# Kernel optimization log

Hardware: AMD Instinct MI355X
Metric: run time of the kernel (lower is better)

## Reference

```python
import jax, jax.numpy as jnp
import numpy as np

EMBED_DIM = 256
NUM_HEADS = 8
WINDOW = 64
HEAD_DIM = EMBED_DIM // NUM_HEADS


def setup_inputs() -> dict:
    key = jax.random.key(0)
    k_x, k_w, k_ow = jax.random.split(key, 3)
    B, S, E = 2, 4096, EMBED_DIM
    x = jax.random.normal(k_x, (B, S, E), dtype=jnp.float32)
    # nn.MultiheadAttention params: packed in_proj (q,k,v) and out_proj
    bound = 1.0 / np.sqrt(E)
    in_proj_w = jax.random.uniform(k_w, (3 * E, E), jnp.float32, -bound, bound)
    in_proj_b = jnp.zeros((3 * E,), jnp.float32)
    out_w = jax.random.uniform(k_ow, (E, E), jnp.float32, -bound, bound)
    out_b = jnp.zeros((E,), jnp.float32)
    return {"x": x, "in_proj_w": in_proj_w, "in_proj_b": in_proj_b,
            "out_w": out_w, "out_b": out_b}


def reference(x, in_proj_w, in_proj_b, out_w, out_b):
    B, S, E = x.shape
    H, D = NUM_HEADS, HEAD_DIM
    # packed qkv projection (torch Linear: y = x @ W^T + b)
    qkv = jnp.einsum('bse,fe->bsf', x, in_proj_w) + in_proj_b  # [B,S,3E]
    q, k, v = jnp.split(qkv, 3, axis=-1)
    q = q.reshape(B, S, H, D).transpose(0, 2, 1, 3)  # [B,H,S,D]
    k = k.reshape(B, S, H, D).transpose(0, 2, 1, 3)
    v = v.reshape(B, S, H, D).transpose(0, 2, 1, 3)
    scale = 1.0 / jnp.sqrt(jnp.asarray(D, x.dtype))
    scores = jnp.einsum('bhqd,bhkd->bhqk', q * scale, k)  # [B,H,S,S]
    idx = jnp.arange(S)
    band = jnp.abs(idx[:, None] - idx[None, :]) <= WINDOW  # [S,S]
    neg = jnp.asarray(-1e9, scores.dtype)
    scores = jnp.where(band[None, None, :, :], scores, neg)
    attn = jax.nn.softmax(scores, axis=-1)
    out = jnp.einsum('bhqk,bhkd->bhqd', attn, v)  # [B,H,S,D]
    out = out.transpose(0, 2, 1, 3).reshape(B, S, E)
    return jnp.einsum('bse,fe->bsf', out, out_w) + out_b
```

## Files before the change

### kernel.cpp

```cpp
#include <hip/hip_runtime.h>
#include <hip/hip_bf16.h>

#define S_LEN 4096
#define EMB   256
#define NHEAD 8
#define HDIM  32
#define WIN   64
#define BATCH 2

typedef __attribute__((ext_vector_type(8))) short short8;
typedef __attribute__((ext_vector_type(4))) float floatx4;
typedef __attribute__((ext_vector_type(4))) unsigned short ushort4v;
typedef unsigned short u16;
typedef unsigned int   u32;

static __device__ __forceinline__ u32 bf16_rn(float x) {
    u32 u = __float_as_uint(x);
    return (u + 0x7FFFu + ((u >> 16) & 1u)) >> 16;
}

static __device__ __forceinline__ void gload16(const u16* g, u16* l) {
    __builtin_amdgcn_global_load_lds(
        (const __attribute__((address_space(1))) void*)g,
        (__attribute__((address_space(3))) void*)l, 16, 0, 0);
}

#define NX4 524288
#define NW4 49152
#define NO4 16384

__global__ __launch_bounds__(256) void convert_kernel(
    const float* __restrict__ X, const float* __restrict__ Wi, const float* __restrict__ Wo,
    u16* __restrict__ Xh, u16* __restrict__ Xl,
    u16* __restrict__ Wih, u16* __restrict__ Wil,
    u16* __restrict__ Woh, u16* __restrict__ Wol)
{
    const int i = blockIdx.x * 256 + threadIdx.x;
    const float* src; u16 *dh, *dl; int off;
    if (i < NX4)            { src = X;  dh = Xh;  dl = Xl;  off = i; }
    else if (i < NX4 + NW4) { src = Wi; dh = Wih; dl = Wil; off = i - NX4; }
    else                    { src = Wo; dh = Woh; dl = Wol; off = i - NX4 - NW4; }
    const float4 v = *(const float4*)(src + (size_t)off * 4);
    ushort4v h, l;
    {
        u32 hb;
        hb = bf16_rn(v.x); h.x = (u16)hb; l.x = (u16)bf16_rn(v.x - __uint_as_float(hb << 16));
        hb = bf16_rn(v.y); h.y = (u16)hb; l.y = (u16)bf16_rn(v.y - __uint_as_float(hb << 16));
        hb = bf16_rn(v.z); h.z = (u16)hb; l.z = (u16)bf16_rn(v.z - __uint_as_float(hb << 16));
        hb = bf16_rn(v.w); h.w = (u16)hb; l.w = (u16)bf16_rn(v.w - __uint_as_float(hb << 16));
    }
    *(ushort4v*)(dh + (size_t)off * 4) = h;
    *(ushort4v*)(dl + (size_t)off * 4) = l;
}

#define BK 32

__global__ __launch_bounds__(256) void qkv_proj_kernel(
    const u16* __restrict__ Xh, const u16* __restrict__ Xl,
    const u16* __restrict__ Wh, const u16* __restrict__ Wl,
    const float* __restrict__ bias,
    u16* __restrict__ Qh, u16* __restrict__ Ql,
    u16* __restrict__ Kh, u16* __restrict__ Kl,
    u16* __restrict__ Vh)
{
    __shared__ __align__(16) u16 SA[2][2][128 * BK];
    __shared__ __align__(16) u16 SB[2][2][64 * BK];

    const int tid = threadIdx.x;
    const int wg0 = blockIdx.y * 12 + blockIdx.x;
    const int wg = (wg0 & 7) * 96 + (wg0 >> 3);
    const int n0 = (wg % 12) * 64, m0 = (wg / 12) * 128;
    const int lane = tid & 63, wv = tid >> 6;
    const int lm = lane & 15, kq = lane >> 4;
    const int gr = lane >> 2;
    const int gc = ((lane & 3) ^ ((lane >> 3) & 3)) * 8;
    const int swz = (lm >> 1) & 3;
    const int wm = (wv >> 1) * 64, wn = (wv & 1) * 32;

    auto stage = [&](int buf, int k0) {
#pragma unroll
        for (int cc = 0; cc < 2; ++cc) {
            const int c = 2 * wv + cc;
            const size_t grow = (size_t)(m0 + 16 * c + gr) * EMB + k0 + gc;
            gload16(Xh + grow, &SA[buf][0][c * 512]);
            gload16(Xl + grow, &SA[buf][1][c * 512]);
        }
        const size_t brow = (size_t)(n0 + 16 * wv + gr) * EMB + k0 + gc;
        gload16(Wh + brow, &SB[buf][0][wv * 512]);
        gload16(Wl + brow, &SB[buf][1][wv * 512]);
    };

    floatx4 acc[4][2] = {};
    stage(0, 0);
    __syncthreads();
    int cur = 0;
    for (int t = 0; t < 8; ++t) {
        if (t < 7) stage(cur ^ 1, (t + 1) * 32);
        short8 a_h[4], a_l[4], b_h[2], b_l[2];
#pragma unroll
        for (int mt = 0; mt < 4; ++mt) {
            const int ro = (wm + mt * 16 + lm) * BK + (kq ^ swz) * 8;
            a_h[mt] = *(const short8*)&SA[cur][0][ro];
            a_l[mt] = *(const short8*)&SA[cur][1][ro];
        }
#pragma unroll
        for (int nt = 0; nt < 2; ++nt) {
            const int ro = (wn + nt * 16 + lm) * BK + (kq ^ swz) * 8;
            b_h[nt] = *(const short8*)&SB[cur][0][ro];
            b_l[nt] = *(const short8*)&SB[cur][1][ro];
        }
#pragma unroll
        for (int mt = 0; mt < 4; ++mt)
#pragma unroll
            for (int nt = 0; nt < 2; ++nt) {
                acc[mt][nt] = __builtin_amdgcn_mfma_f32_16x16x32_bf16(a_h[mt], b_h[nt], acc[mt][nt], 0, 0, 0);
                acc[mt][nt] = __builtin_amdgcn_mfma_f32_16x16x32_bf16(a_h[mt], b_l[nt], acc[mt][nt], 0, 0, 0);
                acc[mt][nt] = __builtin_amdgcn_mfma_f32_16x16x32_bf16(a_l[mt], b_h[nt], acc[mt][nt], 0, 0, 0);
            }
        __syncthreads();
        cur ^= 1;
    }
#pragma unroll
    for (int nt = 0; nt < 2; ++nt) {
        const int f = n0 + wn + nt * 16 + lm;
        const int which = f >> 8;
        const int hh = (f & 255) >> 5, d = f & 31;
        u16* dh = (which == 0) ? Qh : ((which == 1) ? Kh : Vh);
        u16* dl = (which == 0) ? Ql : Kl;
        const float sc2 = (which == 0) ? 0.17677669529663687f : 1.0f;
        const float bf = bias[f];
#pragma unroll
        for (int mt = 0; mt < 4; ++mt)
#pragma unroll
            for (int r = 0; r < 4; ++r) {
                const int m = m0 + wm + mt * 16 + kq * 4 + r;
                const int b = m >> 12, s = m & (S_LEN - 1);
                const size_t idx = (((size_t)b * NHEAD + hh) * S_LEN + s) * HDIM + d;
                const float val = (acc[mt][nt][r] + bf) * sc2;
                const u32 hbits = bf16_rn(val);
                dh[idx] = (u16)hbits;
                if (which != 2)
                    dl[idx] = (u16)bf16_rn(val - __uint_as_float(hbits << 16));
            }
    }
}

__global__ __launch_bounds__(256) void out_proj_kernel(
    const u16* __restrict__ Ahp, const u16* __restrict__ Alp,
    const u16* __restrict__ Wh, const u16* __restrict__ Wl,
    const float* __restrict__ bias, float* __restrict__ C)
{
    __shared__ __align__(16) u16 SA[2][2][64 * BK];
    __shared__ __align__(16) u16 SB[2][2][64 * BK];
    const int tid = threadIdx.x;
    const int wg0 = blockIdx.y * 4 + blockIdx.x;
    const int wg = (wg0 & 7) * 64 + (wg0 >> 3);
    const int n0 = (wg & 3) * 64, m0 = (wg >> 2) * 64;
    const int lane = tid & 63, wv = tid >> 6;
    const int lm = lane & 15, kq = lane >> 4;
    const int gr = lane >> 2;
    const int gc = ((lane & 3) ^ ((lane >> 3) & 3)) * 8;
    const int swz = (lm >> 1) & 3;
    const int wm = (wv >> 1) * 32, wn = (wv & 1) * 32;

    auto stage = [&](int buf, int k0) {
        const size_t arow = (size_t)(m0 + 16 * wv + gr) * EMB + k0 + gc;
        gload16(Ahp + arow, &SA[buf][0][wv * 512]);
        gload16(Alp + arow, &SA[buf][1][wv * 512]);
        const size_t brow = (size_t)(n0 + 16 * wv + gr) * EMB + k0 + gc;
        gload16(Wh + brow, &SB[buf][0][wv * 512]);
        gload16(Wl + brow, &SB[buf][1][wv * 512]);
    };

    floatx4 acc[2][2] = {};
    stage(0, 0);
    __syncthreads();
    int cur = 0;
    for (int t = 0; t < 8; ++t) {
        if (t < 7) stage(cur ^ 1, (t + 1) * 32);
        short8 a_h[2], a_l[2], b_h[2], b_l[2];
#pragma unroll
        for (int mt = 0; mt < 2; ++mt) {
            const int ro = (wm + mt * 16 + lm) * BK + (kq ^ swz) * 8;
            a_h[mt] = *(const short8*)&SA[cur][0][ro];
            a_l[mt] = *(const short8*)&SA[cur][1][ro];
        }
#pragma unroll
        for (int nt = 0; nt < 2; ++nt) {
            const int ro = (wn + nt * 16 + lm) * BK + (kq ^ swz) * 8;
            b_h[nt] = *(const short8*)&SB[cur][0][ro];
            b_l[nt] = *(const short8*)&SB[cur][1][ro];
        }
#pragma unroll
        for (int mt = 0; mt < 2; ++mt)
#pragma unroll
            for (int nt = 0; nt < 2; ++nt) {
                acc[mt][nt] = __builtin_amdgcn_mfma_f32_16x16x32_bf16(a_h[mt], b_h[nt], acc[mt][nt], 0, 0, 0);
                acc[mt][nt] = __builtin_amdgcn_mfma_f32_16x16x32_bf16(a_h[mt], b_l[nt], acc[mt][nt], 0, 0, 0);
                acc[mt][nt] = __builtin_amdgcn_mfma_f32_16x16x32_bf16(a_l[mt], b_h[nt], acc[mt][nt], 0, 0, 0);
            }
        __syncthreads();
        cur ^= 1;
    }
#pragma unroll
    for (int nt = 0; nt < 2; ++nt) {
        const int f = n0 + wn + nt * 16 + lm;
        const float bf = bias[f];
#pragma unroll
        for (int mt = 0; mt < 2; ++mt)
#pragma unroll
            for (int r = 0; r < 4; ++r) {
                const int m = m0 + wm + mt * 16 + kq * 4 + r;
                C[(size_t)m * EMB + f] = acc[mt][nt][r] + bf;
            }
    }
}

#define AKS 40
#define AVS 200

__global__ __launch_bounds__(256) void local_attn_kernel(
    const u16* __restrict__ Qhg, const u16* __restrict__ Qlg,
    const u16* __restrict__ Khg, const u16* __restrict__ Klg,
    const u16* __restrict__ Vhg,
    u16* __restrict__ Abh, u16* __restrict__ Abl)
{
    __shared__ __align__(16) u16 sKh[192 * AKS], sKl[192 * AKS];
    __shared__ __align__(16) u16 sVt[32 * AVS];

    const int tid = threadIdx.x;
    const int q0 = blockIdx.x * 64;
    const int h = blockIdx.y, b = blockIdx.z;
    const int jmin = max(0, q0 - WIN);
    const int jmax = min(S_LEN - 1, q0 + 63 + WIN);
    const int nk = jmax - jmin + 1;
    const size_t bhS = ((size_t)b * NHEAD + h) * S_LEN;
    const size_t qoff = (bhS + q0) * HDIM;
    const size_t koff = (bhS + jmin) * HDIM;

    const int lane = tid & 63, wv = tid >> 6;
    const int lm = lane & 15, quad = lane >> 4;
    const int qbase = wv * 16;

    const short8 qh = *(const short8*)(Qhg + qoff + (size_t)(qbase + lm) * HDIM + quad * 8);
    const short8 ql = *(const short8*)(Qlg + qoff + (size_t)(qbase + lm) * HDIM + quad * 8);

    const int srow = tid >> 2, sc = tid & 3;
#pragma unroll
    for (int r = 0; r < 3; ++r) {
        const int t = srow + r * 64;
        const int tc = min(t, nk - 1);
        const size_t go = koff + (size_t)tc * HDIM + sc * 8;
        *(short8*)&sKh[t * AKS + sc * 8] = *(const short8*)(Khg + go);
        *(short8*)&sKl[t * AKS + sc * 8] = *(const short8*)(Klg + go);
    }
#pragma unroll
    for (int r = 0; r < 3; ++r) {
        const int t = srow + r * 64;
        const int tc = min(t, nk - 1);
        const short8 v = *(const short8*)(Vhg + koff + (size_t)tc * HDIM + sc * 8);
        const int d0 = sc * 8;
#pragma unroll
        for (int j = 0; j < 8; ++j)
            sVt[(d0 + j) * AVS + t] = (u16)v[j];
    }
    __syncthreads();

    const int tb = max(0, ((wv >> 1) << 1) + (min(q0 - WIN, 0) >> 4));

    floatx4 sacc[10];
#pragma unroll
    for (int i = 0; i < 10; ++i) {
        const int nt = tb + i;
        const short8 kh = *(const short8*)&sKh[(nt * 16 + lm) * AKS + quad * 8];
        const short8 kl = *(const short8*)&sKl[(nt * 16 + lm) * AKS + quad * 8];
        floatx4 a = {};
        a = __builtin_amdgcn_mfma_f32_16x16x32_bf16(kh, qh, a, 0, 0, 0);
        a = __builtin_amdgcn_mfma_f32_16x16x32_bf16(kh, ql, a, 0, 0, 0);
        a = __builtin_amdgcn_mfma_f32_16x16x32_bf16(kl, qh, a, 0, 0, 0);
        sacc[i] = a;
    }

    const int qr = q0 + qbase + lm;
    float mx = -1e30f;
#pragma unroll
    for (int i = 0; i < 10; ++i) {
        const int sbase = (tb + i) * 16 + quad * 4;
#pragma unroll
        for (int r = 0; r < 4; ++r) {
            const int slot = sbase + r;
            const int keyg = jmin + slot;
            const bool valid = (slot < nk) && (keyg >= qr - WIN) && (keyg <= qr + WIN);
            const float sv = valid ? sacc[i][r] : -1e30f;
            sacc[i][r] = sv;
            mx = fmaxf(mx, sv);
        }
    }
    mx = fmaxf(mx, __shfl_xor(mx, 16));
    mx = fmaxf(mx, __shfl_xor(mx, 32));

    float l = 0.f;
    u32 pk_[20];
#pragma unroll
    for (int i = 0; i < 10; ++i) {
        const float p0 = __expf(sacc[i][0] - mx);
        const float p1 = __expf(sacc[i][1] - mx);
        const float p2 = __expf(sacc[i][2] - mx);
        const float p3 = __expf(sacc[i][3] - mx);
        l += (p0 + p1) + (p2 + p3);
        pk_[2 * i]     = bf16_rn(p0) | (bf16_rn(p1) << 16);
        pk_[2 * i + 1] = bf16_rn(p2) | (bf16_rn(p3) << 16);
    }
    l += __shfl_xor(l, 16);
    l += __shfl_xor(l, 32);
    const float rl = 1.f / l;

    const int kb = tb >> 1;
    floatx4 oacc[2] = {};
#pragma unroll
    for (int i = 0; i < 5; ++i) {
        const int ks = kb + i;
        uint4 aw;
        aw.x = pk_[4 * i + 0];
        aw.y = pk_[4 * i + 1];
        aw.z = pk_[4 * i + 2];
        aw.w = pk_[4 * i + 3];
        const short8 ap = *(const short8*)&aw;
        const int sb = ks * 32 + quad * 4;
        const uint2 e0 = *(const uint2*)&sVt[lm * AVS + sb];
        const uint2 o0 = *(const uint2*)&sVt[lm * AVS + sb + 16];
        const uint2 e1 = *(const uint2*)&sVt[(16 + lm) * AVS + sb];
        const uint2 o1 = *(const uint2*)&sVt[(16 + lm) * AVS + sb + 16];
        uint4 bw0; bw0.x = e0.x; bw0.y = e0.y; bw0.z = o0.x; bw0.w = o0.y;
        uint4 bw1; bw1.x = e1.x; bw1.y = e1.y; bw1.z = o1.x; bw1.w = o1.y;
        const short8 bv0 = *(const short8*)&bw0;
        const short8 bv1 = *(const short8*)&bw1;
        oacc[0] = __builtin_amdgcn_mfma_f32_16x16x32_bf16(ap, bv0, oacc[0], 0, 0, 0);
        oacc[1] = __builtin_amdgcn_mfma_f32_16x16x32_bf16(ap, bv1, oacc[1], 0, 0, 0);
    }

    float rlr[4];
#pragma unroll
    for (int r = 0; r < 4; ++r) rlr[r] = __shfl(rl, quad * 4 + r);
#pragma unroll
    for (int nt = 0; nt < 2; ++nt)
#pragma unroll
        for (int r = 0; r < 4; ++r) {
            const int qrow = qbase + quad * 4 + r;
            const float o = oacc[nt][r] * rlr[r];
            const u32 hb = bf16_rn(o);
            const size_t idx = ((size_t)b * S_LEN + q0 + qrow) * EMB + h * HDIM + nt * 16 + lm;
            Abh[idx] = (u16)hb;
            Abl[idx] = (u16)bf16_rn(o - __uint_as_float(hb << 16));
        }
}

extern "C" void kernel_launch(void* const* d_in, const int* in_sizes, int n_in,
                              void* d_out, int out_size, void* d_ws, size_t ws_size,
                              hipStream_t stream) {
    const float* x  = (const float*)d_in[0];
    const float* wi = (const float*)d_in[1];
    const float* bi = (const float*)d_in[2];
    const float* wo = (const float*)d_in[3];
    const float* bo = (const float*)d_in[4];
    float* out = (float*)d_out;

    const size_t per = (size_t)BATCH * NHEAD * S_LEN * HDIM;
    u16* p = (u16*)d_ws;
    u16* Xh  = p; p += per;
    u16* Xl  = p; p += per;
    u16* Wih = p; p += 768 * EMB;
    u16* Wil = p; p += 768 * EMB;
    u16* Woh = p; p += EMB * EMB;
    u16* Wol = p; p += EMB * EMB;
    u16* Qh  = p; p += per;
    u16* Ql  = p; p += per;
    u16* Kh  = p; p += per;
    u16* Kl  = p; p += per;
    u16* Vh  = p; p += per;
    u16* Abh = p; p += per;
    u16* Abl = p; p += per;

    convert_kernel<<<dim3((NX4 + NW4 + NO4) / 256), 256, 0, stream>>>(
        x, wi, wo, Xh, Xl, Wih, Wil, Woh, Wol);
    qkv_proj_kernel<<<dim3(768 / 64, 8192 / 128), 256, 0, stream>>>(
        Xh, Xl, Wih, Wil, bi, Qh, Ql, Kh, Kl, Vh);
    local_attn_kernel<<<dim3(S_LEN / 64, NHEAD, BATCH), 256, 0, stream>>>(
        Qh, Ql, Kh, Kl, Vh, Abh, Abl);
    out_proj_kernel<<<dim3(256 / 64, 8192 / 64), 256, 0, stream>>>(
        Abh, Abl, Woh, Wol, bo, out);
}
```

Measured before the change: 108.2 us.

## Store V pre-transposed from QKV projection and load K via swizzled direct-to-LDS copies

```diff
diff --git a/kernel.cpp b/kernel.cpp
--- a/kernel.cpp
+++ b/kernel.cpp
@@ -125,7 +125,7 @@
         const int f = n0 + wn + nt * 16 + lm;
         const int which = f >> 8;
         const int hh = (f & 255) >> 5, d = f & 31;
-        u16* dh = (which == 0) ? Qh : ((which == 1) ? Kh : Vh);
+        u16* dh = (which == 0) ? Qh : Kh;
         u16* dl = (which == 0) ? Ql : Kl;
         const float sc2 = (which == 0) ? 0.17677669529663687f : 1.0f;
         const float bf = bias[f];
@@ -135,12 +135,15 @@
             for (int r = 0; r < 4; ++r) {
                 const int m = m0 + wm + mt * 16 + kq * 4 + r;
                 const int b = m >> 12, s = m & (S_LEN - 1);
-                const size_t idx = (((size_t)b * NHEAD + hh) * S_LEN + s) * HDIM + d;
                 const float val = (acc[mt][nt][r] + bf) * sc2;
                 const u32 hbits = bf16_rn(val);
-                dh[idx] = (u16)hbits;
-                if (which != 2)
+                if (which == 2) {
+                    Vh[((size_t)(b * NHEAD + hh) * HDIM + d) * S_LEN + s] = (u16)hbits;
+                } else {
+                    const size_t idx = (((size_t)b * NHEAD + hh) * S_LEN + s) * HDIM + d;
+                    dh[idx] = (u16)hbits;
                     dl[idx] = (u16)bf16_rn(val - __uint_as_float(hbits << 16));
+                }
             }
     }
 }
@@ -216,13 +219,13 @@
     }
 }
 
-#define AKS 40
+#define AKS 32
 #define AVS 200
 
-__global__ __launch_bounds__(256) void local_attn_kernel(
+__global__ __launch_bounds__(256, 4) void local_attn_kernel(
     const u16* __restrict__ Qhg, const u16* __restrict__ Qlg,
     const u16* __restrict__ Khg, const u16* __restrict__ Klg,
-    const u16* __restrict__ Vhg,
+    const u16* __restrict__ Vtg,
     u16* __restrict__ Abh, u16* __restrict__ Abl)
 {
     __shared__ __align__(16) u16 sKh[192 * AKS], sKl[192 * AKS];
@@ -245,41 +248,45 @@
     const short8 qh = *(const short8*)(Qhg + qoff + (size_t)(qbase + lm) * HDIM + quad * 8);
     const short8 ql = *(const short8*)(Qlg + qoff + (size_t)(qbase + lm) * HDIM + quad * 8);
 
-    const int srow = tid >> 2, sc = tid & 3;
-#pragma unroll
-    for (int r = 0; r < 3; ++r) {
-        const int t = srow + r * 64;
-        const int tc = min(t, nk - 1);
-        const size_t go = koff + (size_t)tc * HDIM + sc * 8;
-        *(short8*)&sKh[t * AKS + sc * 8] = *(const short8*)(Khg + go);
-        *(short8*)&sKl[t * AKS + sc * 8] = *(const short8*)(Klg + go);
-    }
-#pragma unroll
-    for (int r = 0; r < 3; ++r) {
-        const int t = srow + r * 64;
-        const int tc = min(t, nk - 1);
-        const short8 v = *(const short8*)(Vhg + koff + (size_t)tc * HDIM + sc * 8);
-        const int d0 = sc * 8;
-#pragma unroll
-        for (int j = 0; j < 8; ++j)
-            sVt[(d0 + j) * AVS + t] = (u16)v[j];
+    const int gr = lane >> 2;
+    const int gcol = ((lane & 3) ^ ((lane >> 3) & 3)) * 8;
+#pragma unroll
+    for (int cc = 0; cc < 3; ++cc) {
+        const int c = wv * 3 + cc;
+        const int srcrow = min(16 * c + gr, nk - 1);
+        const size_t go = koff + (size_t)srcrow * HDIM + gcol;
+        gload16(Khg + go, &sKh[c * 512]);
+        gload16(Klg + go, &sKl[c * 512]);
+    }
+    const size_t vrow0 = (size_t)((b * NHEAD + h) * HDIM) * S_LEN;
+#pragma unroll
+    for (int p = 0; p < 3; ++p) {
+        const int c = tid + p * 256;
+        const int d = c / 24, t8 = (c % 24) * 8;
+        const int ss = min(jmin + t8, S_LEN - 8);
+        const short8 v = *(const short8*)(Vtg + vrow0 + (size_t)d * S_LEN + ss);
+        *(short8*)&sVt[d * AVS + t8] = v;
     }
     __syncthreads();
 
     const int tb = max(0, ((wv >> 1) << 1) + (min(q0 - WIN, 0) >> 4));
+    const int swz = (lm >> 1) & 3;
 
     floatx4 sacc[10];
+    __builtin_amdgcn_s_setprio(1);
 #pragma unroll
     for (int i = 0; i < 10; ++i) {
         const int nt = tb + i;
-        const short8 kh = *(const short8*)&sKh[(nt * 16 + lm) * AKS + quad * 8];
-        const short8 kl = *(const short8*)&sKl[(nt * 16 + lm) * AKS + quad * 8];
+        const int ro = (nt * 16 + lm) * AKS + (quad ^ swz) * 8;
+        const short8 kh = *(const short8*)&sKh[ro];
+        const short8 kl = *(const short8*)&sKl[ro];
         floatx4 a = {};
         a = __builtin_amdgcn_mfma_f32_16x16x32_bf16(kh, qh, a, 0, 0, 0);
         a = __builtin_amdgcn_mfma_f32_16x16x32_bf16(kh, ql, a, 0, 0, 0);
         a = __builtin_amdgcn_mfma_f32_16x16x32_bf16(kl, qh, a, 0, 0, 0);
         sacc[i] = a;
     }
+    __builtin_amdgcn_s_setprio(0);
 
     const int qr = q0 + qbase + lm;
     float mx = -1e30f;
@@ -317,6 +324,7 @@
 
     const int kb = tb >> 1;
     floatx4 oacc[2] = {};
+    __builtin_amdgcn_s_setprio(1);
 #pragma unroll
     for (int i = 0; i < 5; ++i) {
         const int ks = kb + i;
@@ -338,6 +346,7 @@
         oacc[0] = __builtin_amdgcn_mfma_f32_16x16x32_bf16(ap, bv0, oacc[0], 0, 0, 0);
         oacc[1] = __builtin_amdgcn_mfma_f32_16x16x32_bf16(ap, bv1, oacc[1], 0, 0, 0);
     }
+    __builtin_amdgcn_s_setprio(0);
 
     float rlr[4];
 #pragma unroll
@@ -377,16 +386,16 @@
     u16* Ql  = p; p += per;
     u16* Kh  = p; p += per;
     u16* Kl  = p; p += per;
-    u16* Vh  = p; p += per;
+    u16* Vt  = p; p += per;
     u16* Abh = p; p += per;
     u16* Abl = p; p += per;
 
     convert_kernel<<<dim3((NX4 + NW4 + NO4) / 256), 256, 0, stream>>>(
         x, wi, wo, Xh, Xl, Wih, Wil, Woh, Wol);
     qkv_proj_kernel<<<dim3(768 / 64, 8192 / 128), 256, 0, stream>>>(
-        Xh, Xl, Wih, Wil, bi, Qh, Ql, Kh, Kl, Vh);
+        Xh, Xl, Wih, Wil, bi, Qh, Ql, Kh, Kl, Vt);
     local_attn_kernel<<<dim3(S_LEN / 64, NHEAD, BATCH), 256, 0, stream>>>(
-        Qh, Ql, Kh, Kl, Vh, Abh, Abl);
+        Qh, Ql, Kh, Kl, Vt, Abh, Abl);
     out_proj_kernel<<<dim3(256 / 64, 8192 / 64), 256, 0, stream>>>(
         Abh, Abl, Woh, Wol, bo, out);
 }
```

Result: slower. 111.6 us (+3.2%).
